# Performance work log

Hardware: AMD Instinct MI355X
Metric: run time of the kernel (lower is better)

The kernel has to match this reference:

```python
import jax, jax.numpy as jnp
import numpy as np

EPS = 1e-7  # K.epsilon()
NUM_CAPSULE = 32
DIM_CAPSULE = 16
ROUTINGS = 3


def squash(x, axis=-1):
    # NOTE: this repo's squash is pure L2 normalization (no |s|^2/(1+|s|^2) factor)
    s2 = jnp.sum(jnp.square(x), axis=axis, keepdims=True)
    return x / jnp.sqrt(s2 + EPS)


def setup_inputs() -> dict:
    key = jax.random.key(0)
    k1, k2 = jax.random.split(key)
    B, L, D_IN = 32, 2048, 64
    u_vecs = jax.random.normal(k1, (B, L, D_IN), dtype=jnp.float32)
    # glorot-ish scale for the capsule kernel
    W = jax.random.normal(k2, (1, D_IN, NUM_CAPSULE * DIM_CAPSULE), dtype=jnp.float32) * 0.05
    return {"u_vecs": u_vecs, "W": W}


def reference(u_vecs, W):
    B, L, _ = u_vecs.shape
    # K.conv1d with kernel size 1 == pointwise matmul
    u_hat = jnp.einsum('bli,io->blo', u_vecs, W[0])
    u_hat = u_hat.reshape(B, L, NUM_CAPSULE, DIM_CAPSULE)
    u_hat = jnp.transpose(u_hat, (0, 2, 1, 3))  # [B, nc, L, dc]

    b = jnp.zeros((B, NUM_CAPSULE, L), dtype=u_hat.dtype)
    outputs = None
    for i in range(ROUTINGS):
        # softmax over the num_capsule axis (axis=1), per the permute dance in the source
        c = jax.nn.softmax(b, axis=1)  # [B, nc, L]
        outputs = squash(jnp.einsum('bnl,bnld->bnd', c, u_hat))  # [B, nc, dc]
        if i < ROUTINGS - 1:
            b = jnp.einsum('bnd,bnld->bnl', outputs, u_hat)  # overwrite, not accumulate
    return outputs
```

## Files before the change

kernel.cpp:

```cpp
#include <hip/hip_runtime.h>

#define NC 32
#define DC 16
#define LSEQ 2048

__global__ __launch_bounds__(256) void k_sum_u(const float* __restrict__ u,
                                               float* __restrict__ v0p) {
    int b  = blockIdx.x >> 3;
    int l0 = (blockIdx.x & 7) * 256;
    int q  = threadIdx.x & 15;
    int r  = threadIdx.x >> 4;
    const float4* u4 = (const float4*)u;
    float4 acc = {0.f, 0.f, 0.f, 0.f};
#pragma unroll
    for (int j = 0; j < 16; ++j) {
        int l = l0 + r + 16 * j;
        float4 x = u4[(b * LSEQ + l) * 16 + q];
        acc.x += x.x; acc.y += x.y; acc.z += x.z; acc.w += x.w;
    }
    __shared__ float red[16][64];
    red[r][q * 4 + 0] = acc.x;
    red[r][q * 4 + 1] = acc.y;
    red[r][q * 4 + 2] = acc.z;
    red[r][q * 4 + 3] = acc.w;
    __syncthreads();
    if (threadIdx.x < 64) {
        float s = 0.f;
#pragma unroll
        for (int rr = 0; rr < 16; ++rr) s += red[rr][threadIdx.x];
        v0p[blockIdx.x * 64 + threadIdx.x] = s;
    }
}

template <bool BCAST, bool FINAL>
__global__ __launch_bounds__(64) void k_caps(const float* __restrict__ v,
                                             const float* __restrict__ W,
                                             float* __restrict__ wtil,
                                             float* __restrict__ out,
                                             float vscale) {
    int b  = blockIdx.x >> 3;
    int ng = blockIdx.x & 7;
    int t  = threadIdx.x;
    __shared__ float vS[4][72];
    __shared__ float oS[4][16];
    if (BCAST) {
        float s = 0.f;
#pragma unroll
        for (int ch = 0; ch < 8; ++ch) s += v[(b * 8 + ch) * 64 + t];
        s *= vscale;
#pragma unroll
        for (int n4 = 0; n4 < 4; ++n4) vS[n4][t] = s;
    } else {
        int row = t >> 4, col4 = t & 15;
        const float4* v4 = (const float4*)v;
        float4 a = {0.f, 0.f, 0.f, 0.f};
#pragma unroll
        for (int ch = 0; ch < 16; ++ch) {
            float4 x = v4[(b * 16 + ch) * 512 + (ng * 4 + row) * 16 + col4];
            a.x += x.x; a.y += x.y; a.z += x.z; a.w += x.w;
        }
        ((float4*)&vS[row][0])[col4] = a;
    }
    __syncthreads();
    int n4 = t >> 4, d = t & 15;
    int n  = ng * 4 + n4;
    const float* vrow = &vS[n4][0];
    float s = 0.f;
#pragma unroll
    for (int i = 0; i < 64; ++i)
        s = fmaf(vrow[i], W[i * (NC * DC) + n * DC + d], s);
    float s2 = s * s;
#pragma unroll
    for (int off = 8; off >= 1; off >>= 1) s2 += __shfl_xor(s2, off, 16);
    float o = s / sqrtf(s2 + 1e-7f);
    if (FINAL) {
        out[b * (NC * DC) + n * DC + d] = o;
    } else {
        oS[n4][d] = o;
        __syncthreads();
        int i4 = t & 15;
        float4 wv;
        float* wvp = (float*)&wv;
#pragma unroll
        for (int k = 0; k < 4; ++k) {
            int i = i4 * 4 + k;
            float acc = 0.f;
#pragma unroll
            for (int dd = 0; dd < 16; ++dd)
                acc = fmaf(W[i * (NC * DC) + n * DC + dd], oS[n4][dd], acc);
            wvp[k] = acc;
        }
        ((float4*)wtil)[(b * (NC * 64) + n * 64 + i4 * 4) >> 2] = wv;
    }
}

__global__ __launch_bounds__(128) void k_route(const float* __restrict__ u,
                                               const float* __restrict__ wtil,
                                               float* __restrict__ vpart) {
    int b    = blockIdx.x >> 4;
    int ch   = blockIdx.x & 15;
    int l0   = ch * 128;
    int t    = threadIdx.x;
    int w    = t >> 6;
    int lane = t & 63;
    int lr   = lane & 7;
    int lc   = lane >> 3;
    int dr   = lane & 7;
    int nc   = lane >> 3;

    __shared__ float uS[128 * 68];
    __shared__ float wS[32 * 68];
    __shared__ float cS[2 * 2304];
    float4* uS4 = (float4*)uS;
    float4* wS4 = (float4*)wS;
    float*  cw  = cS + w * 2304;
    float4* cw4 = (float4*)cw;

    const float4* ug = (const float4*)(u + (b * LSEQ + l0) * 64);
#pragma unroll
    for (int r = 0; r < 16; ++r) {
        int idx = t + 128 * r;
        uS4[(idx >> 4) * 17 + (idx & 15)] = ug[idx];
    }
    const float4* wg = (const float4*)(wtil + b * (NC * 64));
#pragma unroll
    for (int r = 0; r < 4; ++r) {
        int idx = t + 128 * r;
        wS4[(idx >> 4) * 17 + (idx & 15)] = wg[idx];
    }
    __syncthreads();

    float acc[8][4];
#pragma unroll
    for (int i = 0; i < 8; ++i)
#pragma unroll
        for (int j = 0; j < 4; ++j) acc[i][j] = 0.f;
    int arow = w * 64 + lr;
#pragma unroll 4
    for (int k4 = 0; k4 < 16; ++k4) {
        float4 wf[4];
#pragma unroll
        for (int j = 0; j < 4; ++j) wf[j] = wS4[(lc * 4 + j) * 17 + k4];
#pragma unroll
        for (int i = 0; i < 8; ++i) {
            float4 a = uS4[(arow + 8 * i) * 17 + k4];
#pragma unroll
            for (int j = 0; j < 4; ++j) {
                acc[i][j] = fmaf(a.x, wf[j].x, acc[i][j]);
                acc[i][j] = fmaf(a.y, wf[j].y, acc[i][j]);
                acc[i][j] = fmaf(a.z, wf[j].z, acc[i][j]);
                acc[i][j] = fmaf(a.w, wf[j].w, acc[i][j]);
            }
        }
    }

#pragma unroll
    for (int i = 0; i < 8; ++i) {
        float m = fmaxf(fmaxf(acc[i][0], acc[i][1]), fmaxf(acc[i][2], acc[i][3]));
        m = fmaxf(m, __shfl_xor(m, 8));
        m = fmaxf(m, __shfl_xor(m, 16));
        m = fmaxf(m, __shfl_xor(m, 32));
        float e0 = __expf(acc[i][0] - m), e1 = __expf(acc[i][1] - m);
        float e2 = __expf(acc[i][2] - m), e3 = __expf(acc[i][3] - m);
        float ss = e0 + e1 + e2 + e3;
        ss += __shfl_xor(ss, 8);
        ss += __shfl_xor(ss, 16);
        ss += __shfl_xor(ss, 32);
        float inv = 1.f / ss;
        float4 cvv = {e0 * inv, e1 * inv, e2 * inv, e3 * inv};
        cw4[(lr + 8 * i) * 9 + lc] = cvv;
    }
    __syncthreads();

    float vacc[4][8];
#pragma unroll
    for (int j = 0; j < 4; ++j)
#pragma unroll
        for (int k = 0; k < 8; ++k) vacc[j][k] = 0.f;
#pragma unroll 8
    for (int lrel = 0; lrel < 64; ++lrel) {
        float4 cv = cw4[lrel * 9 + nc];
        const float4* ur = uS4 + (w * 64 + lrel) * 17 + dr * 2;
        float4 u0 = ur[0], u1 = ur[1];
        float* cp = (float*)&cv;
#pragma unroll
        for (int j = 0; j < 4; ++j) {
            float c = cp[j];
            vacc[j][0] = fmaf(c, u0.x, vacc[j][0]);
            vacc[j][1] = fmaf(c, u0.y, vacc[j][1]);
            vacc[j][2] = fmaf(c, u0.z, vacc[j][2]);
            vacc[j][3] = fmaf(c, u0.w, vacc[j][3]);
            vacc[j][4] = fmaf(c, u1.x, vacc[j][4]);
            vacc[j][5] = fmaf(c, u1.y, vacc[j][5]);
            vacc[j][6] = fmaf(c, u1.z, vacc[j][6]);
            vacc[j][7] = fmaf(c, u1.w, vacc[j][7]);
        }
    }

#pragma unroll
    for (int j = 0; j < 4; ++j) {
        float* rp = cw + (nc * 4 + j) * 64 + dr * 8;
        float4 r0 = {vacc[j][0], vacc[j][1], vacc[j][2], vacc[j][3]};
        float4 r1 = {vacc[j][4], vacc[j][5], vacc[j][6], vacc[j][7]};
        ((float4*)rp)[0] = r0;
        ((float4*)rp)[1] = r1;
    }
    __syncthreads();
    float4* cS4 = (float4*)cS;
    float4* vp4 = (float4*)(vpart + blockIdx.x * 2048);
#pragma unroll
    for (int s = 0; s < 4; ++s) {
        int idx4 = t + 128 * s;
        float4 a = cS4[idx4];
        float4 c2 = cS4[576 + idx4];
        float4 o = {a.x + c2.x, a.y + c2.y, a.z + c2.z, a.w + c2.w};
        vp4[idx4] = o;
    }
}

extern "C" void kernel_launch(void* const* d_in, const int* in_sizes, int n_in,
                              void* d_out, int out_size, void* d_ws, size_t ws_size,
                              hipStream_t stream) {
    const float* u = (const float*)d_in[0];
    const float* W = (const float*)d_in[1];
    float* out = (float*)d_out;
    float* ws  = (float*)d_ws;
    float* v0p   = ws;
    float* wt    = ws + 16384;
    float* vpart = ws + 16384 + 65536;

    k_sum_u<<<256, 256, 0, stream>>>(u, v0p);
    k_caps<true, false><<<256, 64, 0, stream>>>(v0p, W, wt, nullptr, 1.0f / 32.0f);
    k_route<<<512, 128, 0, stream>>>(u, wt, vpart);
    k_caps<false, false><<<256, 64, 0, stream>>>(vpart, W, wt, nullptr, 1.0f);
    k_route<<<512, 128, 0, stream>>>(u, wt, vpart);
    k_caps<false, true><<<256, 64, 0, stream>>>(vpart, W, nullptr, out, 1.0f);
}
```

Measured before the change: 108.3 us.

## Fuse capsule squash and W-tilde computation into routing kernel

Removes the two intermediate k_caps launches by having every routing block recompute the per-batch capsule outputs and the W·o projection from the reduced partials in shared memory. The routing kernel moves to 256 threads with 4 waves each handling 32 positions, and the partial sums are combined through a shared-memory tree reduction. The launch count drops from six to four, but each of the 16 blocks per batch now repeats the capsule and W-tilde arithmetic and rereads W and the partials, which is redundant work.

```diff
diff --git a/kernel.cpp b/kernel.cpp
--- a/kernel.cpp
+++ b/kernel.cpp
@@ -1,11 +1,11 @@
 #include <hip/hip_runtime.h>
 
+#define LSEQ 2048
 #define NC 32
 #define DC 16
-#define LSEQ 2048
 
 __global__ __launch_bounds__(256) void k_sum_u(const float* __restrict__ u,
-                                               float* __restrict__ v0p) {
+                                               float* __restrict__ part0) {
     int b  = blockIdx.x >> 3;
     int l0 = (blockIdx.x & 7) * 256;
     int q  = threadIdx.x & 15;
@@ -28,121 +28,115 @@
         float s = 0.f;
 #pragma unroll
         for (int rr = 0; rr < 16; ++rr) s += red[rr][threadIdx.x];
-        v0p[blockIdx.x * 64 + threadIdx.x] = s;
+        part0[blockIdx.x * 64 + threadIdx.x] = s;
     }
 }
 
-template <bool BCAST, bool FINAL>
-__global__ __launch_bounds__(64) void k_caps(const float* __restrict__ v,
-                                             const float* __restrict__ W,
-                                             float* __restrict__ wtil,
-                                             float* __restrict__ out,
-                                             float vscale) {
-    int b  = blockIdx.x >> 3;
-    int ng = blockIdx.x & 7;
-    int t  = threadIdx.x;
-    __shared__ float vS[4][72];
-    __shared__ float oS[4][16];
-    if (BCAST) {
-        float s = 0.f;
-#pragma unroll
-        for (int ch = 0; ch < 8; ++ch) s += v[(b * 8 + ch) * 64 + t];
-        s *= vscale;
-#pragma unroll
-        for (int n4 = 0; n4 < 4; ++n4) vS[n4][t] = s;
-    } else {
-        int row = t >> 4, col4 = t & 15;
-        const float4* v4 = (const float4*)v;
-        float4 a = {0.f, 0.f, 0.f, 0.f};
-#pragma unroll
-        for (int ch = 0; ch < 16; ++ch) {
-            float4 x = v4[(b * 16 + ch) * 512 + (ng * 4 + row) * 16 + col4];
-            a.x += x.x; a.y += x.y; a.z += x.z; a.w += x.w;
-        }
-        ((float4*)&vS[row][0])[col4] = a;
-    }
-    __syncthreads();
-    int n4 = t >> 4, d = t & 15;
-    int n  = ng * 4 + n4;
-    const float* vrow = &vS[n4][0];
-    float s = 0.f;
-#pragma unroll
-    for (int i = 0; i < 64; ++i)
-        s = fmaf(vrow[i], W[i * (NC * DC) + n * DC + d], s);
-    float s2 = s * s;
-#pragma unroll
-    for (int off = 8; off >= 1; off >>= 1) s2 += __shfl_xor(s2, off, 16);
-    float o = s / sqrtf(s2 + 1e-7f);
-    if (FINAL) {
-        out[b * (NC * DC) + n * DC + d] = o;
-    } else {
-        oS[n4][d] = o;
-        __syncthreads();
-        int i4 = t & 15;
-        float4 wv;
-        float* wvp = (float*)&wv;
-#pragma unroll
-        for (int k = 0; k < 4; ++k) {
-            int i = i4 * 4 + k;
-            float acc = 0.f;
-#pragma unroll
-            for (int dd = 0; dd < 16; ++dd)
-                acc = fmaf(W[i * (NC * DC) + n * DC + dd], oS[n4][dd], acc);
-            wvp[k] = acc;
-        }
-        ((float4*)wtil)[(b * (NC * 64) + n * 64 + i4 * 4) >> 2] = wv;
-    }
-}
-
-__global__ __launch_bounds__(128) void k_route(const float* __restrict__ u,
-                                               const float* __restrict__ wtil,
-                                               float* __restrict__ vpart) {
-    int b    = blockIdx.x >> 4;
-    int ch   = blockIdx.x & 15;
-    int l0   = ch * 128;
-    int t    = threadIdx.x;
-    int w    = t >> 6;
-    int lane = t & 63;
-    int lr   = lane & 7;
-    int lc   = lane >> 3;
-    int dr   = lane & 7;
-    int nc   = lane >> 3;
+template <int MODE>
+__global__ __launch_bounds__(256, 2) void k_route(
+    const float* __restrict__ u,
+    const float* __restrict__ W,
+    const float* __restrict__ vsrc,
+    float* __restrict__ vout)
+{
+    const int bid  = blockIdx.x;
+    const int b    = bid >> 4;
+    const int ch   = bid & 15;
+    const int t    = threadIdx.x;
+    const int w    = t >> 6;
+    const int lane = t & 63;
+    const int lr   = lane & 7;
+    const int lc   = lane >> 3;
 
     __shared__ float uS[128 * 68];
     __shared__ float wS[32 * 68];
-    __shared__ float cS[2 * 2304];
+    __shared__ float cR[4096];
     float4* uS4 = (float4*)uS;
     float4* wS4 = (float4*)wS;
-    float*  cw  = cS + w * 2304;
-    float4* cw4 = (float4*)cw;
-
-    const float4* ug = (const float4*)(u + (b * LSEQ + l0) * 64);
-#pragma unroll
-    for (int r = 0; r < 16; ++r) {
-        int idx = t + 128 * r;
+    float4* cR4 = (float4*)cR;
+
+    const float4* ug = (const float4*)(u + (b * LSEQ + ch * 128) * 64);
+#pragma unroll
+    for (int r = 0; r < 8; ++r) {
+        int idx = t + 256 * r;
         uS4[(idx >> 4) * 17 + (idx & 15)] = ug[idx];
     }
-    const float4* wg = (const float4*)(wtil + b * (NC * 64));
-#pragma unroll
-    for (int r = 0; r < 4; ++r) {
-        int idx = t + 128 * r;
-        wS4[(idx >> 4) * 17 + (idx & 15)] = wg[idx];
-    }
-    __syncthreads();
-
-    float acc[8][4];
-#pragma unroll
-    for (int i = 0; i < 8; ++i)
+
+    if (MODE == 0) {
+        if (t < 64) {
+            float s = 0.f;
+#pragma unroll
+            for (int c2 = 0; c2 < 8; ++c2) s += vsrc[(b * 8 + c2) * 64 + t];
+            cR[t] = s * (1.0f / 32.0f);
+        }
+    } else {
+#pragma unroll
+        for (int r = 0; r < 8; ++r) {
+            int e = t + 256 * r;
+            float s = 0.f;
+#pragma unroll
+            for (int c2 = 0; c2 < 16; ++c2) s += vsrc[(b * 16 + c2) * 2048 + e];
+            cR[(e >> 6) * 65 + (e & 63)] = s;
+        }
+    }
+    __syncthreads();
+
+    float* oS = cR + 2112;
+    {
+        int n0 = t >> 4;
+        const float* va = (MODE == 0) ? cR : (cR + n0 * 65);
+        const float* vb = (MODE == 0) ? cR : (cR + (n0 + 16) * 65);
+        float s0 = 0.f, s1 = 0.f;
+#pragma unroll
+        for (int i = 0; i < 64; ++i) {
+            float w0 = W[i * 512 + t];
+            float w1 = W[i * 512 + 256 + t];
+            s0 = fmaf(va[i], w0, s0);
+            s1 = fmaf(vb[i], w1, s1);
+        }
+        float q0 = s0 * s0, q1 = s1 * s1;
+#pragma unroll
+        for (int off = 1; off <= 8; off <<= 1) {
+            q0 += __shfl_xor(q0, off);
+            q1 += __shfl_xor(q1, off);
+        }
+        int d = t & 15;
+        oS[n0 * 17 + d]        = s0 / sqrtf(q0 + 1e-7f);
+        oS[(n0 + 16) * 17 + d] = s1 / sqrtf(q1 + 1e-7f);
+    }
+    __syncthreads();
+
+#pragma unroll
+    for (int r = 0; r < 8; ++r) {
+        int e = t + 256 * r;
+        int n = e & 31, i = e >> 5;
+        const float4* Wr = (const float4*)(W + i * 512 + n * 16);
+        float a = 0.f;
+#pragma unroll
+        for (int q = 0; q < 4; ++q) {
+            float4 wv = Wr[q];
+            a = fmaf(wv.x, oS[n * 17 + 4 * q + 0], a);
+            a = fmaf(wv.y, oS[n * 17 + 4 * q + 1], a);
+            a = fmaf(wv.z, oS[n * 17 + 4 * q + 2], a);
+            a = fmaf(wv.w, oS[n * 17 + 4 * q + 3], a);
+        }
+        wS[n * 68 + i] = a;
+    }
+    __syncthreads();
+
+    float acc[4][4];
+#pragma unroll
+    for (int i = 0; i < 4; ++i)
 #pragma unroll
         for (int j = 0; j < 4; ++j) acc[i][j] = 0.f;
-    int arow = w * 64 + lr;
+    const int arow = w * 32 + lr;
 #pragma unroll 4
     for (int k4 = 0; k4 < 16; ++k4) {
         float4 wf[4];
 #pragma unroll
-        for (int j = 0; j < 4; ++j) wf[j] = wS4[(lc * 4 + j) * 17 + k4];
-#pragma unroll
-        for (int i = 0; i < 8; ++i) {
+        for (int j = 0; j < 4; ++j) wf[j] = wS4[(lc + 8 * j) * 17 + k4];
+#pragma unroll
+        for (int i = 0; i < 4; ++i) {
             float4 a = uS4[(arow + 8 * i) * 17 + k4];
 #pragma unroll
             for (int j = 0; j < 4; ++j) {
@@ -155,20 +149,22 @@
     }
 
 #pragma unroll
-    for (int i = 0; i < 8; ++i) {
+    for (int i = 0; i < 4; ++i) {
         float m = fmaxf(fmaxf(acc[i][0], acc[i][1]), fmaxf(acc[i][2], acc[i][3]));
         m = fmaxf(m, __shfl_xor(m, 8));
         m = fmaxf(m, __shfl_xor(m, 16));
         m = fmaxf(m, __shfl_xor(m, 32));
-        float e0 = __expf(acc[i][0] - m), e1 = __expf(acc[i][1] - m);
-        float e2 = __expf(acc[i][2] - m), e3 = __expf(acc[i][3] - m);
+        float e0 = __expf(acc[i][0] - m);
+        float e1 = __expf(acc[i][1] - m);
+        float e2 = __expf(acc[i][2] - m);
+        float e3 = __expf(acc[i][3] - m);
         float ss = e0 + e1 + e2 + e3;
         ss += __shfl_xor(ss, 8);
         ss += __shfl_xor(ss, 16);
         ss += __shfl_xor(ss, 32);
         float inv = 1.f / ss;
-        float4 cvv = {e0 * inv, e1 * inv, e2 * inv, e3 * inv};
-        cw4[(lr + 8 * i) * 9 + lc] = cvv;
+        float4 cv = {e0 * inv, e1 * inv, e2 * inv, e3 * inv};
+        cR4[(arow + 8 * i) * 8 + lc] = cv;
     }
     __syncthreads();
 
@@ -177,12 +173,13 @@
     for (int j = 0; j < 4; ++j)
 #pragma unroll
         for (int k = 0; k < 8; ++k) vacc[j][k] = 0.f;
-#pragma unroll 8
-    for (int lrel = 0; lrel < 64; ++lrel) {
-        float4 cv = cw4[lrel * 9 + nc];
-        const float4* ur = uS4 + (w * 64 + lrel) * 17 + dr * 2;
-        float4 u0 = ur[0], u1 = ur[1];
-        float* cp = (float*)&cv;
+#pragma unroll 4
+    for (int lrel = 0; lrel < 32; ++lrel) {
+        int l = w * 32 + lrel;
+        float4 cv = cR4[l * 8 + lc];
+        float4 u0 = uS4[l * 17 + lr * 2];
+        float4 u1 = uS4[l * 17 + lr * 2 + 1];
+        const float* cp = (const float*)&cv;
 #pragma unroll
         for (int j = 0; j < 4; ++j) {
             float c = cp[j];
@@ -196,26 +193,94 @@
             vacc[j][7] = fmaf(c, u1.w, vacc[j][7]);
         }
     }
-
-#pragma unroll
-    for (int j = 0; j < 4; ++j) {
-        float* rp = cw + (nc * 4 + j) * 64 + dr * 8;
-        float4 r0 = {vacc[j][0], vacc[j][1], vacc[j][2], vacc[j][3]};
-        float4 r1 = {vacc[j][4], vacc[j][5], vacc[j][6], vacc[j][7]};
-        ((float4*)rp)[0] = r0;
-        ((float4*)rp)[1] = r1;
-    }
-    __syncthreads();
-    float4* cS4 = (float4*)cS;
-    float4* vp4 = (float4*)(vpart + blockIdx.x * 2048);
-#pragma unroll
-    for (int s = 0; s < 4; ++s) {
-        int idx4 = t + 128 * s;
-        float4 a = cS4[idx4];
-        float4 c2 = cS4[576 + idx4];
-        float4 o = {a.x + c2.x, a.y + c2.y, a.z + c2.z, a.w + c2.w};
-        vp4[idx4] = o;
-    }
+    __syncthreads();
+
+    if (w >= 2) {
+        float4* red = cR4 + (w - 2) * 512;
+#pragma unroll
+        for (int j = 0; j < 4; ++j) {
+            int n = lc + 8 * j;
+            float4 r0 = {vacc[j][0], vacc[j][1], vacc[j][2], vacc[j][3]};
+            float4 r1 = {vacc[j][4], vacc[j][5], vacc[j][6], vacc[j][7]};
+            red[n * 16 + lr * 2]     = r0;
+            red[n * 16 + lr * 2 + 1] = r1;
+        }
+    }
+    __syncthreads();
+    if (w < 2) {
+        const float4* red = cR4 + w * 512;
+#pragma unroll
+        for (int j = 0; j < 4; ++j) {
+            int n = lc + 8 * j;
+            float4 r0 = red[n * 16 + lr * 2];
+            float4 r1 = red[n * 16 + lr * 2 + 1];
+            vacc[j][0] += r0.x; vacc[j][1] += r0.y;
+            vacc[j][2] += r0.z; vacc[j][3] += r0.w;
+            vacc[j][4] += r1.x; vacc[j][5] += r1.y;
+            vacc[j][6] += r1.z; vacc[j][7] += r1.w;
+        }
+    }
+    __syncthreads();
+    if (w == 1) {
+        float4* red = cR4 + 512;
+#pragma unroll
+        for (int j = 0; j < 4; ++j) {
+            int n = lc + 8 * j;
+            float4 r0 = {vacc[j][0], vacc[j][1], vacc[j][2], vacc[j][3]};
+            float4 r1 = {vacc[j][4], vacc[j][5], vacc[j][6], vacc[j][7]};
+            red[n * 16 + lr * 2]     = r0;
+            red[n * 16 + lr * 2 + 1] = r1;
+        }
+    }
+    __syncthreads();
+    if (w == 0) {
+        const float4* red = cR4 + 512;
+        float4* out4 = (float4*)(vout + bid * 2048);
+#pragma unroll
+        for (int j = 0; j < 4; ++j) {
+            int n = lc + 8 * j;
+            float4 r0 = red[n * 16 + lr * 2];
+            float4 r1 = red[n * 16 + lr * 2 + 1];
+            float4 o0 = {vacc[j][0] + r0.x, vacc[j][1] + r0.y,
+                         vacc[j][2] + r0.z, vacc[j][3] + r0.w};
+            float4 o1 = {vacc[j][4] + r1.x, vacc[j][5] + r1.y,
+                         vacc[j][6] + r1.z, vacc[j][7] + r1.w};
+            out4[n * 16 + lr * 2]     = o0;
+            out4[n * 16 + lr * 2 + 1] = o1;
+        }
+    }
+}
+
+__global__ __launch_bounds__(64) void k_caps_final(const float* __restrict__ v,
+                                                   const float* __restrict__ W,
+                                                   float* __restrict__ out) {
+    int b  = blockIdx.x >> 3;
+    int ng = blockIdx.x & 7;
+    int t  = threadIdx.x;
+    __shared__ float vS[4][72];
+    {
+        int row = t >> 4, col4 = t & 15;
+        const float4* v4 = (const float4*)v;
+        float4 a = {0.f, 0.f, 0.f, 0.f};
+#pragma unroll
+        for (int c2 = 0; c2 < 16; ++c2) {
+            float4 x = v4[(b * 16 + c2) * 512 + (ng * 4 + row) * 16 + col4];
+            a.x += x.x; a.y += x.y; a.z += x.z; a.w += x.w;
+        }
+        ((float4*)&vS[row][0])[col4] = a;
+    }
+    __syncthreads();
+    int n4 = t >> 4, d = t & 15;
+    int n  = ng * 4 + n4;
+    const float* vrow = &vS[n4][0];
+    float s = 0.f;
+#pragma unroll
+    for (int i = 0; i < 64; ++i)
+        s = fmaf(vrow[i], W[i * (NC * DC) + n * DC + d], s);
+    float s2 = s * s;
+#pragma unroll
+    for (int off = 8; off >= 1; off >>= 1) s2 += __shfl_xor(s2, off, 16);
+    out[b * (NC * DC) + n * DC + d] = s / sqrtf(s2 + 1e-7f);
 }
 
 extern "C" void kernel_launch(void* const* d_in, const int* in_sizes, int n_in,
@@ -225,14 +290,12 @@
     const float* W = (const float*)d_in[1];
     float* out = (float*)d_out;
     float* ws  = (float*)d_ws;
-    float* v0p   = ws;
-    float* wt    = ws + 16384;
-    float* vpart = ws + 16384 + 65536;
-
-    k_sum_u<<<256, 256, 0, stream>>>(u, v0p);
-    k_caps<true, false><<<256, 64, 0, stream>>>(v0p, W, wt, nullptr, 1.0f / 32.0f);
-    k_route<<<512, 128, 0, stream>>>(u, wt, vpart);
-    k_caps<false, false><<<256, 64, 0, stream>>>(vpart, W, wt, nullptr, 1.0f);
-    k_route<<<512, 128, 0, stream>>>(u, wt, vpart);
-    k_caps<false, true><<<256, 64, 0, stream>>>(vpart, W, nullptr, out, 1.0f);
+    float* part0  = ws;
+    float* vpartA = ws + 16384;
+    float* vpartB = vpartA + 512 * 2048;
+
+    k_sum_u<<<256, 256, 0, stream>>>(u, part0);
+    k_route<0><<<512, 256, 0, stream>>>(u, W, part0, vpartA);
+    k_route<1><<<512, 256, 0, stream>>>(u, W, vpartA, vpartB);
+    k_caps_final<<<256, 64, 0, stream>>>(vpartB, W, out);
 }
```

Result: no change. 109.0 us (+0.6%).
